# Optimization experiments

Hardware: AMD Instinct MI355X
Metric: run time of the kernel (lower is better)

The kernel has to match this reference:

```python
import jax, jax.numpy as jnp
import numpy as np

N, DIM, EDGE_DIM, HEADS, EXP_HEADS, E = 50000, 64, 32, 8, 16, 800000
HEAD_DIM = DIM // HEADS
SCALE = HEAD_DIM ** -0.5
EPS = 1e-16


def setup_inputs() -> dict:
    key = jax.random.key(0)
    ks = jax.random.split(key, 16)
    s = DIM ** -0.5
    return {
        "x": jax.random.normal(ks[0], (N, DIM), jnp.float32),
        "edges": jax.random.normal(ks[1], (E, EDGE_DIM), jnp.float32),
        "edge_index": jax.random.randint(ks[2], (2, E), 0, N, jnp.int64),
        "Wq": jax.random.normal(ks[3], (DIM, DIM), jnp.float32) * s,
        "Wk": jax.random.normal(ks[4], (DIM, DIM), jnp.float32) * s,
        "Wv": jax.random.normal(ks[5], (DIM, DIM), jnp.float32) * s,
        "Wek": jax.random.normal(ks[6], (EDGE_DIM, DIM), jnp.float32) * (EDGE_DIM ** -0.5),
        "Wev": jax.random.normal(ks[7], (EDGE_DIM, DIM), jnp.float32) * (EDGE_DIM ** -0.5),
        "Wexp": jax.random.normal(ks[8], (HEADS, EXP_HEADS), jnp.float32) * (HEADS ** -0.5),
        "Wsq": jax.random.normal(ks[9], (EXP_HEADS, HEADS), jnp.float32) * (EXP_HEADS ** -0.5),
        "bsq": jax.random.normal(ks[10], (HEADS,), jnp.float32) * 0.01,
        "Wout": jax.random.normal(ks[11], (DIM, DIM), jnp.float32) * s,
        "bout": jax.random.normal(ks[12], (DIM,), jnp.float32) * 0.01,
        "temperature": jnp.full((1,), 0.01, jnp.float32),
    }


def reference(x, edges, edge_index, Wq, Wk, Wv, Wek, Wev, Wexp, Wsq, bsq, Wout, bout, temperature):
    n = x.shape[0]
    dst = edge_index[0]  # segment / query index
    src = edge_index[1]  # key/value gather index

    q = (x @ Wq).reshape(n, HEADS, HEAD_DIM)      # [n,h,d]
    k = (x @ Wk).reshape(n, HEADS, HEAD_DIM)
    v = (x @ Wv).reshape(n, HEADS, HEAD_DIM)      # v_non_scatter

    qe = q[dst]                                   # [E,h,d] edge gathers
    ke = k[src]
    ve = v[src]

    edge_k = (edges @ Wek).reshape(-1, HEADS, HEAD_DIM)
    edge_v = (edges @ Wev).reshape(-1, HEADS, HEAD_DIM)

    ke = (ke + edge_k) * SCALE
    attn = jnp.einsum('ehd,ehd->eh', qe, ke) / temperature[0]  # [E,h]
    attn = attn @ Wexp                                          # [E,eh]

    # sparse (segment) softmax over edges grouped by dst, per expanded head
    mx = jax.ops.segment_max(attn, dst, num_segments=n)         # [n,eh]
    ex = jnp.exp(attn - mx[dst])
    sm = jax.ops.segment_sum(ex, dst, num_segments=n)
    attn = ex / (sm[dst] + EPS)

    attn = attn @ Wsq + bsq                                     # [E,h]

    ve = ve + edge_v
    out_e = attn[:, :, None] * ve                               # [E,h,d]
    agg = jax.ops.segment_sum(out_e, dst, num_segments=n)       # [n,h,d]

    out = (v - agg).reshape(n, DIM)                             # graph Laplacian: v - aggregated
    out = out @ Wout + bout
    return out, attn.T  # attention returned as [h, E]
```

## Files before the change

kernel.cpp:

```cpp
#include <hip/hip_runtime.h>
#include <hip/hip_fp16.h>

#define N_NODES 50000
#define DIM 64
#define EDGE_DIM 32
#define HEADS 8
#define EXP_HEADS 16
#define NEDGE 800000
#define SCALE 0.35355339059327373f
#define EPS 1e-16f
#define NEG_BIG -1e30f
#define NB_SCAN ((N_NODES + 255) / 256)

#define RFL(x) __builtin_amdgcn_readfirstlane(x)

__device__ __forceinline__ float h2f(unsigned short u) {
    __half h;
    *reinterpret_cast<unsigned short*>(&h) = u;
    return __half2float(h);
}
__device__ __forceinline__ unsigned short f2h(float f) {
    __half h = __float2half(f);
    return *reinterpret_cast<unsigned short*>(&h);
}

__global__ __launch_bounds__(256) void qkv_kernel(
    const float* __restrict__ x, const float* __restrict__ Wq,
    const float* __restrict__ Wk, const float* __restrict__ Wv,
    float* __restrict__ q, unsigned short* __restrict__ kh,
    float* __restrict__ v, unsigned short* __restrict__ vh) {
    int gid = blockIdx.x * 256 + threadIdx.x;
    if (gid >= (N_NODES / 4) * DIM) return;
    int quad = gid >> 6, j = gid & 63;
    long i0 = (long)quad * 4;
    float aq[4] = {0,0,0,0}, ak[4] = {0,0,0,0}, av[4] = {0,0,0,0};
#pragma unroll
    for (int l = 0; l < DIM; ++l) {
        float wq = Wq[l * DIM + j], wk = Wk[l * DIM + j], wv = Wv[l * DIM + j];
#pragma unroll
        for (int r = 0; r < 4; ++r) {
            float xv = x[(i0 + r) * DIM + l];
            aq[r] = fmaf(xv, wq, aq[r]);
            ak[r] = fmaf(xv, wk, ak[r]);
            av[r] = fmaf(xv, wv, av[r]);
        }
    }
#pragma unroll
    for (int r = 0; r < 4; ++r) {
        q[(i0 + r) * DIM + j] = aq[r];
        kh[(i0 + r) * DIM + j] = f2h(ak[r]);
        v[(i0 + r) * DIM + j] = av[r];
        vh[(i0 + r) * DIM + j] = f2h(av[r]);
    }
}

__global__ __launch_bounds__(256) void hist_kernel(
    const int* __restrict__ eidx, unsigned* __restrict__ cnt) {
    int e = blockIdx.x * 256 + threadIdx.x;
    if (e >= NEDGE) return;
    atomicAdd(&cnt[eidx[e]], 1u);
}

__global__ __launch_bounds__(256) void scan_reduce(
    const unsigned* __restrict__ cnt, unsigned* __restrict__ blocksum) {
    int gid = blockIdx.x * 256 + threadIdx.x;
    unsigned v = (gid < N_NODES) ? cnt[gid] : 0u;
    v += __shfl_xor(v, 1);  v += __shfl_xor(v, 2);
    v += __shfl_xor(v, 4);  v += __shfl_xor(v, 8);
    v += __shfl_xor(v, 16); v += __shfl_xor(v, 32);
    __shared__ unsigned ws4[4];
    if ((threadIdx.x & 63) == 0) ws4[threadIdx.x >> 6] = v;
    __syncthreads();
    if (threadIdx.x == 0)
        blocksum[blockIdx.x] = ws4[0] + ws4[1] + ws4[2] + ws4[3];
}

__global__ __launch_bounds__(256) void scan_base(
    const unsigned* __restrict__ blocksum, unsigned* __restrict__ blockbase) {
    __shared__ unsigned ps[256];
    int t = threadIdx.x;
    unsigned v = (t < NB_SCAN) ? blocksum[t] : 0u;
    ps[t] = v;
    __syncthreads();
    for (int off = 1; off < 256; off <<= 1) {
        unsigned val = (t >= off) ? ps[t - off] : 0u;
        __syncthreads();
        ps[t] += val;
        __syncthreads();
    }
    blockbase[t] = ps[t] - v;
}

__global__ __launch_bounds__(256) void scan_final(
    const unsigned* __restrict__ cnt, const unsigned* __restrict__ blockbase,
    unsigned* __restrict__ offsets, unsigned* __restrict__ cursor) {
    __shared__ unsigned ps[256];
    int t = threadIdx.x;
    int gid = blockIdx.x * 256 + t;
    unsigned v = (gid < N_NODES) ? cnt[gid] : 0u;
    ps[t] = v;
    __syncthreads();
    for (int off = 1; off < 256; off <<= 1) {
        unsigned val = (t >= off) ? ps[t - off] : 0u;
        __syncthreads();
        ps[t] += val;
        __syncthreads();
    }
    unsigned off_ = blockbase[blockIdx.x] + ps[t] - v;
    if (gid < N_NODES) { offsets[gid] = off_; cursor[gid] = off_; }
    if (gid == N_NODES - 1) offsets[N_NODES] = off_ + v;
}

__global__ __launch_bounds__(256) void scatter_kernel(
    const int* __restrict__ eidx, const float4* __restrict__ edges4,
    unsigned* __restrict__ cursor,
    unsigned* __restrict__ iperm, unsigned* __restrict__ srcs,
    unsigned short* __restrict__ esort) {
    int e = blockIdx.x * 256 + threadIdx.x;
    if (e >= NEDGE) return;
    int dst = eidx[e];
    unsigned pos = atomicAdd(&cursor[dst], 1u);
    iperm[e] = pos;
    srcs[pos] = (unsigned)eidx[NEDGE + e];
    const float4* src = edges4 + (long)e * 8;
    ushort4* dst4 = (ushort4*)(esort + (long)pos * EDGE_DIM);
#pragma unroll
    for (int i = 0; i < 8; ++i) {
        float4 t = src[i];
        ushort4 o;
        o.x = f2h(t.x); o.y = f2h(t.y); o.z = f2h(t.z); o.w = f2h(t.w);
        dst4[i] = o;
    }
}

__global__ __launch_bounds__(256) void edge_attn_kernel(
    const unsigned short* __restrict__ esort,
    const float* __restrict__ q, const unsigned short* __restrict__ kh,
    const float* __restrict__ Wek,
    const float* __restrict__ temp,
    const unsigned* __restrict__ offsets, const unsigned* __restrict__ srcs,
    float* __restrict__ logit8) {
    int tid = threadIdx.x;
    int w = tid >> 6, lane = tid & 63;
    int h = lane >> 3, d = lane & 7;
    float wekr[4][8];
#pragma unroll
    for (int j = 0; j < 4; ++j)
#pragma unroll
        for (int i = 0; i < 8; ++i)
            wekr[j][i] = Wek[(d * 4 + j) * DIM + h * 8 + i];
    float invt = SCALE / temp[0];
    int n = blockIdx.x * 4 + w;
    unsigned nb = offsets[n];
    int deg = (int)(offsets[n + 1] - nb);
    const float* __restrict__ qp = q + (long)n * DIM;
    float qreg = qp[lane];
    float qv[8];
#pragma unroll
    for (int t = 0; t < 8; ++t) qv[t] = qp[h * 8 + t];
    float g0 = 0.f, g1 = 0.f, g2 = 0.f, g3 = 0.f;
#pragma unroll
    for (int t = 0; t < 8; ++t) {
        g0 = fmaf(qv[t], wekr[0][t], g0);
        g1 = fmaf(qv[t], wekr[1][t], g1);
        g2 = fmaf(qv[t], wekr[2][t], g2);
        g3 = fmaf(qv[t], wekr[3][t], g3);
    }
    int j = 0;
    for (; j + 4 <= deg; j += 4) {
        float p[4];
#pragma unroll
        for (int g2i = 0; g2i < 4; ++g2i) {
            long slot = (long)nb + j + g2i;
            int s_g = RFL((int)srcs[slot]);
            float kv = h2f(kh[(long)s_g * DIM + lane]);
            ushort4 ue = *(const ushort4*)(esort + slot * EDGE_DIM + d * 4);
            float pp = qreg * kv;
            pp = fmaf(g0, h2f(ue.x), pp);
            pp = fmaf(g1, h2f(ue.y), pp);
            pp = fmaf(g2, h2f(ue.z), pp);
            pp = fmaf(g3, h2f(ue.w), pp);
            p[g2i] = pp;
        }
#pragma unroll
        for (int i = 0; i < 4; ++i) p[i] += __shfl_xor(p[i], 1);
#pragma unroll
        for (int i = 0; i < 4; ++i) p[i] += __shfl_xor(p[i], 2);
#pragma unroll
        for (int i = 0; i < 4; ++i) p[i] += __shfl_xor(p[i], 4);
        if (d == 0) {
#pragma unroll
            for (int i = 0; i < 4; ++i)
                logit8[((long)nb + j + i) * HEADS + h] = p[i] * invt;
        }
    }
    for (; j < deg; ++j) {
        long slot = (long)nb + j;
        int s_g = RFL((int)srcs[slot]);
        float kv = h2f(kh[(long)s_g * DIM + lane]);
        ushort4 ue = *(const ushort4*)(esort + slot * EDGE_DIM + d * 4);
        float pp = qreg * kv;
        pp = fmaf(g0, h2f(ue.x), pp);
        pp = fmaf(g1, h2f(ue.y), pp);
        pp = fmaf(g2, h2f(ue.z), pp);
        pp = fmaf(g3, h2f(ue.w), pp);
        pp += __shfl_xor(pp, 1);
        pp += __shfl_xor(pp, 2);
        pp += __shfl_xor(pp, 4);
        if (d == 0) logit8[slot * HEADS + h] = pp * invt;
    }
}

__global__ __launch_bounds__(256) void node_fused_kernel(
    const unsigned short* __restrict__ esort,
    const unsigned short* __restrict__ vh,
    const float* __restrict__ v, const float* __restrict__ logit8,
    const unsigned* __restrict__ offsets,
    const unsigned* __restrict__ srcs,
    const float* __restrict__ Wexp, const float* __restrict__ Wsq,
    const float* __restrict__ bsq, const float* __restrict__ Wev,
    float* __restrict__ a8s, float* __restrict__ vmagg) {
    int tid = threadIdx.x;
    int w = tid >> 6, lane = tid & 63;
    int g = lane >> 4, t16 = lane & 15;
    int h = lane >> 3, d = lane & 7;
    float we[HEADS];
#pragma unroll
    for (int hh = 0; hh < HEADS; ++hh) we[hh] = Wexp[hh * EXP_HEADS + t16];
    float wsq[HEADS];
#pragma unroll
    for (int j = 0; j < HEADS; ++j) wsq[j] = Wsq[t16 * HEADS + j];
    int hmap = 4 * (t16 & 1) + 2 * ((t16 >> 1) & 1) + ((t16 >> 2) & 1);
    int ih = ((h >> 2) & 1) | (((h >> 1) & 1) << 1) | ((h & 1) << 2);
    float bs_h = bsq[h], bs_w = bsq[hmap];
    bool b0 = (t16 & 1), b1 = (t16 & 2), b2 = (t16 & 4);

    int n = blockIdx.x * 4 + w;
    unsigned nb = offsets[n];
    int deg = (int)(offsets[n + 1] - nb);

    float m = NEG_BIG, s = 0.f;
    for (int j0 = 0; j0 < deg; j0 += 4) {
        const float4* lp = (const float4*)(logit8 + ((long)nb + j0 + g) * HEADS);
        float4 l0 = lp[0], l1 = lp[1];
        float a = l0.x * we[0];
        a = fmaf(l0.y, we[1], a); a = fmaf(l0.z, we[2], a); a = fmaf(l0.w, we[3], a);
        a = fmaf(l1.x, we[4], a); a = fmaf(l1.y, we[5], a);
        a = fmaf(l1.z, we[6], a); a = fmaf(l1.w, we[7], a);
        if (j0 + g < deg) {
            float mn = fmaxf(m, a);
            s = s * __expf(m - mn) + __expf(a - mn);
            m = mn;
        }
    }
#pragma unroll
    for (int off = 16; off < 64; off <<= 1) {
        float m2 = __shfl_xor(m, off), s2 = __shfl_xor(s, off);
        float mn = fmaxf(m, m2);
        s = s * __expf(m - mn) + s2 * __expf(m2 - mn);
        m = mn;
    }
    float rs = 1.f / (s + EPS);

    float acc = 0.f, t0 = 0.f, t1 = 0.f, t2 = 0.f, t3 = 0.f;
    for (int j0 = 0; j0 < deg; j0 += 4) {
        int cnt = deg - j0; if (cnt > 4) cnt = 4;
        const float4* lp = (const float4*)(logit8 + ((long)nb + j0 + g) * HEADS);
        float4 l0 = lp[0], l1 = lp[1];
        float a = l0.x * we[0];
        a = fmaf(l0.y, we[1], a); a = fmaf(l0.z, we[2], a); a = fmaf(l0.w, we[3], a);
        a = fmaf(l1.x, we[4], a); a = fmaf(l1.y, we[5], a);
        a = fmaf(l1.z, we[6], a); a = fmaf(l1.w, we[7], a);
        float p = (g < cnt) ? __expf(a - m) * rs : 0.f;
        float v0 = p * wsq[0], v1 = p * wsq[1], v2 = p * wsq[2], v3 = p * wsq[3];
        float v4 = p * wsq[4], v5 = p * wsq[5], v6 = p * wsq[6], v7 = p * wsq[7];
        float q0, q1, q2, q3, n0, n1, s8;
        q0 = (b0 ? v4 : v0) + __shfl_xor(b0 ? v0 : v4, 1);
        q1 = (b0 ? v5 : v1) + __shfl_xor(b0 ? v1 : v5, 1);
        q2 = (b0 ? v6 : v2) + __shfl_xor(b0 ? v2 : v6, 1);
        q3 = (b0 ? v7 : v3) + __shfl_xor(b0 ? v3 : v7, 1);
        n0 = (b1 ? q2 : q0) + __shfl_xor(b1 ? q0 : q2, 2);
        n1 = (b1 ? q3 : q1) + __shfl_xor(b1 ? q1 : q3, 2);
        s8 = (b2 ? n1 : n0) + __shfl_xor(b2 ? n0 : n1, 4);
        float a8sum = s8 + __shfl_xor(s8, 8);
        if (t16 < 8 && g < cnt)
            a8s[((long)nb + j0 + g) * HEADS + hmap] = a8sum + bs_w;
#pragma unroll
        for (int i = 0; i < 4; ++i) {
            if (i < cnt) {
                long slot = (long)nb + j0 + i;
                int s_g = RFL((int)srcs[slot]);
                float a8 = __shfl(a8sum, i * 16 + ih) + bs_h;
                float vv = h2f(vh[(long)s_g * DIM + lane]);
                ushort4 ue = *(const ushort4*)(esort + slot * EDGE_DIM + d * 4);
                acc = fmaf(a8, vv, acc);
                t0 = fmaf(a8, h2f(ue.x), t0);
                t1 = fmaf(a8, h2f(ue.y), t1);
                t2 = fmaf(a8, h2f(ue.z), t2);
                t3 = fmaf(a8, h2f(ue.w), t3);
            }
        }
    }
    float ev = 0.f;
#pragma unroll
    for (int l = 0; l < EDGE_DIM; ++l) {
        float tv = ((l & 3) == 0) ? t0 : ((l & 3) == 1) ? t1 : ((l & 3) == 2) ? t2 : t3;
        float tl = __shfl(tv, h * 8 + (l >> 2));
        ev = fmaf(tl, Wev[l * DIM + lane], ev);
    }
    vmagg[(long)n * DIM + lane] = v[(long)n * DIM + lane] - (acc + ev);
}

__global__ __launch_bounds__(256) void transpose_kernel(
    const float* __restrict__ a8s, const unsigned* __restrict__ iperm,
    float* __restrict__ out2) {
    int e = blockIdx.x * 256 + threadIdx.x;
    if (e >= NEDGE) return;
    long sj = iperm[e];
    const float4* p = (const float4*)(a8s + sj * HEADS);
    float4 lo = p[0], hi = p[1];
    out2[0L * NEDGE + e] = lo.x; out2[1L * NEDGE + e] = lo.y;
    out2[2L * NEDGE + e] = lo.z; out2[3L * NEDGE + e] = lo.w;
    out2[4L * NEDGE + e] = hi.x; out2[5L * NEDGE + e] = hi.y;
    out2[6L * NEDGE + e] = hi.z; out2[7L * NEDGE + e] = hi.w;
}

__global__ __launch_bounds__(256) void out_kernel(
    const float* __restrict__ vmagg, const float* __restrict__ Wout,
    const float* __restrict__ bout, float* __restrict__ out) {
    int gid = blockIdx.x * 256 + threadIdx.x;
    if (gid >= (N_NODES / 4) * DIM) return;
    int quad = gid >> 6, j = gid & 63;
    long i0 = (long)quad * 4;
    float b = bout[j];
    float ac[4] = {b, b, b, b};
#pragma unroll
    for (int l = 0; l < DIM; ++l) {
        float wv = Wout[l * DIM + j];
#pragma unroll
        for (int r = 0; r < 4; ++r)
            ac[r] = fmaf(vmagg[(i0 + r) * DIM + l], wv, ac[r]);
    }
#pragma unroll
    for (int r = 0; r < 4; ++r) out[(i0 + r) * DIM + j] = ac[r];
}

extern "C" void kernel_launch(void* const* d_in, const int* in_sizes, int n_in,
                              void* d_out, int out_size, void* d_ws, size_t ws_size,
                              hipStream_t stream) {
    const float* x     = (const float*)d_in[0];
    const float* edges = (const float*)d_in[1];
    const int*   eidx  = (const int*)d_in[2];
    const float* Wq    = (const float*)d_in[3];
    const float* Wk    = (const float*)d_in[4];
    const float* Wv    = (const float*)d_in[5];
    const float* Wek   = (const float*)d_in[6];
    const float* Wev   = (const float*)d_in[7];
    const float* Wexp  = (const float*)d_in[8];
    const float* Wsq   = (const float*)d_in[9];
    const float* bsq   = (const float*)d_in[10];
    const float* Wout  = (const float*)d_in[11];
    const float* bout  = (const float*)d_in[12];
    const float* temp  = (const float*)d_in[13];

    float* ws = (float*)d_ws;
    float* q       = ws;
    unsigned short* kh = (unsigned short*)(ws + 3200000L);
    float* v       = ws + 6400000L;
    float* logit8  = ws + 9600000L;
    float* vmagg   = ws + 16000000L;
    float* a8s     = q;
    unsigned* iperm     = (unsigned*)(ws + 19200000L);
    unsigned* srcs      = iperm + NEDGE;
    unsigned* cnt       = srcs + NEDGE;
    unsigned* offsets   = cnt + N_NODES;
    unsigned* cursor    = offsets + N_NODES + 1;
    unsigned* blocksum  = cursor + N_NODES;
    unsigned* blockbase = blocksum + 256;
    unsigned short* esort = (unsigned short*)(ws + 21800000L);
    unsigned short* vh    = (unsigned short*)(ws + 34600000L);

    hipMemsetAsync(cnt, 0, (size_t)N_NODES * sizeof(unsigned), stream);

    float* out1 = (float*)d_out;
    float* out2 = out1 + (long)N_NODES * DIM;

    qkv_kernel<<<(N_NODES / 4 * DIM + 255) / 256, 256, 0, stream>>>(x, Wq, Wk, Wv, q, kh, v, vh);
    hist_kernel<<<(NEDGE + 255) / 256, 256, 0, stream>>>(eidx, cnt);
    scan_reduce<<<NB_SCAN, 256, 0, stream>>>(cnt, blocksum);
    scan_base<<<1, 256, 0, stream>>>(blocksum, blockbase);
    scan_final<<<NB_SCAN, 256, 0, stream>>>(cnt, blockbase, offsets, cursor);
    scatter_kernel<<<(NEDGE + 255) / 256, 256, 0, stream>>>(eidx, (const float4*)edges,
                                                            cursor, iperm, srcs, esort);
    edge_attn_kernel<<<N_NODES / 4, 256, 0, stream>>>(esort, q, kh, Wek, temp,
                                                      offsets, srcs, logit8);
    node_fused_kernel<<<N_NODES / 4, 256, 0, stream>>>(esort, vh, v, logit8, offsets, srcs,
                                                       Wexp, Wsq, bsq, Wev, a8s, vmagg);
    transpose_kernel<<<(NEDGE + 255) / 256, 256, 0, stream>>>(a8s, iperm, out2);
    out_kernel<<<(N_NODES / 4 * DIM + 255) / 256, 256, 0, stream>>>(vmagg, Wout, bout, out1);
}
```

Measured before the change: 437.4 us.

## Compute online softmax max/sum stats in edge_attn kernel instead of node pass

```diff
diff --git a/kernel.cpp b/kernel.cpp
--- a/kernel.cpp
+++ b/kernel.cpp
@@ -136,10 +136,10 @@
 __global__ __launch_bounds__(256) void edge_attn_kernel(
     const unsigned short* __restrict__ esort,
     const float* __restrict__ q, const unsigned short* __restrict__ kh,
-    const float* __restrict__ Wek,
+    const float* __restrict__ Wek, const float* __restrict__ Wexp,
     const float* __restrict__ temp,
     const unsigned* __restrict__ offsets, const unsigned* __restrict__ srcs,
-    float* __restrict__ logit8) {
+    float* __restrict__ logit8, float2* __restrict__ stats2) {
     int tid = threadIdx.x;
     int w = tid >> 6, lane = tid & 63;
     int h = lane >> 3, d = lane & 7;
@@ -149,6 +149,8 @@
 #pragma unroll
         for (int i = 0; i < 8; ++i)
             wekr[j][i] = Wek[(d * 4 + j) * DIM + h * 8 + i];
+    float we0 = Wexp[h * EXP_HEADS + 2 * d];
+    float we1 = Wexp[h * EXP_HEADS + 2 * d + 1];
     float invt = SCALE / temp[0];
     int n = blockIdx.x * 4 + w;
     unsigned nb = offsets[n];
@@ -166,6 +168,7 @@
         g2 = fmaf(qv[t], wekr[2][t], g2);
         g3 = fmaf(qv[t], wekr[3][t], g3);
     }
+    float m0 = NEG_BIG, s0 = 0.f, m1 = NEG_BIG, s1 = 0.f;
     int j = 0;
     for (; j + 4 <= deg; j += 4) {
         float p[4];
@@ -188,10 +191,30 @@
         for (int i = 0; i < 4; ++i) p[i] += __shfl_xor(p[i], 2);
 #pragma unroll
         for (int i = 0; i < 4; ++i) p[i] += __shfl_xor(p[i], 4);
+#pragma unroll
+        for (int i = 0; i < 4; ++i) p[i] *= invt;
         if (d == 0) {
 #pragma unroll
             for (int i = 0; i < 4; ++i)
-                logit8[((long)nb + j + i) * HEADS + h] = p[i] * invt;
+                logit8[((long)nb + j + i) * HEADS + h] = p[i];
+        }
+        float c0[4], c1[4];
+#pragma unroll
+        for (int i = 0; i < 4; ++i) { c0[i] = p[i] * we0; c1[i] = p[i] * we1; }
+#pragma unroll
+        for (int i = 0; i < 4; ++i) { c0[i] += __shfl_xor(c0[i], 8);  c1[i] += __shfl_xor(c1[i], 8); }
+#pragma unroll
+        for (int i = 0; i < 4; ++i) { c0[i] += __shfl_xor(c0[i], 16); c1[i] += __shfl_xor(c1[i], 16); }
+#pragma unroll
+        for (int i = 0; i < 4; ++i) { c0[i] += __shfl_xor(c0[i], 32); c1[i] += __shfl_xor(c1[i], 32); }
+#pragma unroll
+        for (int i = 0; i < 4; ++i) {
+            float mn0 = fmaxf(m0, c0[i]);
+            s0 = s0 * __expf(m0 - mn0) + __expf(c0[i] - mn0);
+            m0 = mn0;
+            float mn1 = fmaxf(m1, c1[i]);
+            s1 = s1 * __expf(m1 - mn1) + __expf(c1[i] - mn1);
+            m1 = mn1;
         }
     }
     for (; j < deg; ++j) {
@@ -207,7 +230,24 @@
         pp += __shfl_xor(pp, 1);
         pp += __shfl_xor(pp, 2);
         pp += __shfl_xor(pp, 4);
-        if (d == 0) logit8[slot * HEADS + h] = pp * invt;
+        pp *= invt;
+        if (d == 0) logit8[slot * HEADS + h] = pp;
+        float c0 = pp * we0, c1 = pp * we1;
+        c0 += __shfl_xor(c0, 8);  c1 += __shfl_xor(c1, 8);
+        c0 += __shfl_xor(c0, 16); c1 += __shfl_xor(c1, 16);
+        c0 += __shfl_xor(c0, 32); c1 += __shfl_xor(c1, 32);
+        float mn0 = fmaxf(m0, c0);
+        s0 = s0 * __expf(m0 - mn0) + __expf(c0 - mn0);
+        m0 = mn0;
+        float mn1 = fmaxf(m1, c1);
+        s1 = s1 * __expf(m1 - mn1) + __expf(c1 - mn1);
+        m1 = mn1;
+    }
+    if (h == 0) {
+        float2 st0; st0.x = m0; st0.y = 1.f / (s0 + EPS);
+        float2 st1; st1.x = m1; st1.y = 1.f / (s1 + EPS);
+        stats2[(long)n * EXP_HEADS + 2 * d] = st0;
+        stats2[(long)n * EXP_HEADS + 2 * d + 1] = st1;
     }
 }
 
@@ -216,7 +256,7 @@
     const unsigned short* __restrict__ vh,
     const float* __restrict__ v, const float* __restrict__ logit8,
     const unsigned* __restrict__ offsets,
-    const unsigned* __restrict__ srcs,
+    const unsigned* __restrict__ srcs, const float2* __restrict__ stats2,
     const float* __restrict__ Wexp, const float* __restrict__ Wsq,
     const float* __restrict__ bsq, const float* __restrict__ Wev,
     float* __restrict__ a8s, float* __restrict__ vmagg) {
@@ -239,28 +279,8 @@
     unsigned nb = offsets[n];
     int deg = (int)(offsets[n + 1] - nb);
 
-    float m = NEG_BIG, s = 0.f;
-    for (int j0 = 0; j0 < deg; j0 += 4) {
-        const float4* lp = (const float4*)(logit8 + ((long)nb + j0 + g) * HEADS);
-        float4 l0 = lp[0], l1 = lp[1];
-        float a = l0.x * we[0];
-        a = fmaf(l0.y, we[1], a); a = fmaf(l0.z, we[2], a); a = fmaf(l0.w, we[3], a);
-        a = fmaf(l1.x, we[4], a); a = fmaf(l1.y, we[5], a);
-        a = fmaf(l1.z, we[6], a); a = fmaf(l1.w, we[7], a);
-        if (j0 + g < deg) {
-            float mn = fmaxf(m, a);
-            s = s * __expf(m - mn) + __expf(a - mn);
-            m = mn;
-        }
-    }
-#pragma unroll
-    for (int off = 16; off < 64; off <<= 1) {
-        float m2 = __shfl_xor(m, off), s2 = __shfl_xor(s, off);
-        float mn = fmaxf(m, m2);
-        s = s * __expf(m - mn) + s2 * __expf(m2 - mn);
-        m = mn;
-    }
-    float rs = 1.f / (s + EPS);
+    float2 st = stats2[(long)n * EXP_HEADS + t16];
+    float m = st.x, rs = st.y;
 
     float acc = 0.f, t0 = 0.f, t1 = 0.f, t2 = 0.f, t3 = 0.f;
     for (int j0 = 0; j0 < deg; j0 += 4) {
@@ -379,6 +399,7 @@
     unsigned* blockbase = blocksum + 256;
     unsigned short* esort = (unsigned short*)(ws + 21800000L);
     unsigned short* vh    = (unsigned short*)(ws + 34600000L);
+    float2* stats2 = (float2*)(ws + 36200000L);
 
     hipMemsetAsync(cnt, 0, (size_t)N_NODES * sizeof(unsigned), stream);
 
@@ -392,10 +413,10 @@
     scan_final<<<NB_SCAN, 256, 0, stream>>>(cnt, blockbase, offsets, cursor);
     scatter_kernel<<<(NEDGE + 255) / 256, 256, 0, stream>>>(eidx, (const float4*)edges,
                                                             cursor, iperm, srcs, esort);
-    edge_attn_kernel<<<N_NODES / 4, 256, 0, stream>>>(esort, q, kh, Wek, temp,
-                                                      offsets, srcs, logit8);
+    edge_attn_kernel<<<N_NODES / 4, 256, 0, stream>>>(esort, q, kh, Wek, Wexp, temp,
+                                                      offsets, srcs, logit8, stats2);
     node_fused_kernel<<<N_NODES / 4, 256, 0, stream>>>(esort, vh, v, logit8, offsets, srcs,
-                                                       Wexp, Wsq, bsq, Wev, a8s, vmagg);
+                                                       stats2, Wexp, Wsq, bsq, Wev, a8s, vmagg);
     transpose_kernel<<<(NEDGE + 255) / 256, 256, 0, stream>>>(a8s, iperm, out2);
     out_kernel<<<(N_NODES / 4 * DIM + 255) / 256, 256, 0, stream>>>(vmagg, Wout, bout, out1);
 }
```

After: 438.9 us. No clear change (+0.3%).
